# Performance work log

Measured on AMD Instinct MI355X. Metric: run time of the kernel, lower is better.

## Reference

```python
import jax, jax.numpy as jnp
import numpy as np

B, T, C = 2, 1024, 2048
HEAD_SIZE = 64
H = C // HEAD_SIZE          # 32 heads
N_LAYER, LAYER_ID = 24, 12
D_MIX_LORA = 32
LN_EPS = 1e-5


def _layer_norm(x, g, b):
    mu = jnp.mean(x, axis=-1, keepdims=True)
    var = jnp.mean(jnp.square(x - mu), axis=-1, keepdims=True)
    return (x - mu) * jax.lax.rsqrt(var + LN_EPS) * g + b


def setup_inputs() -> dict:
    key = jax.random.key(0)
    ks = jax.random.split(key, 8)
    # data-dependent init of time_maa_* exactly as in the torch module
    r01 = LAYER_ID / (N_LAYER - 1)
    r1a0 = 1.0 - LAYER_ID / N_LAYER
    ddd = np.arange(C, dtype=np.float32) / C
    time_maa_x = jnp.asarray(1.0 - np.power(ddd, r1a0), dtype=jnp.float32)
    time_maa_r = jnp.asarray(1.0 - np.power(ddd, 0.5 * r1a0), dtype=jnp.float32)
    time_maa_k = jnp.asarray(1.0 - np.power(ddd, r1a0), dtype=jnp.float32)
    time_maa_v = jnp.asarray(1.0 - (np.power(ddd, r1a0) + 0.3 * r01), dtype=jnp.float32)
    # LoRA mix weights (w1 is zero-init in the module, keep small random for a nontrivial test)
    w1 = jax.random.uniform(ks[0], (C, D_MIX_LORA * 3), jnp.float32, -0.01, 0.01)
    w2 = jax.random.uniform(ks[1], (3, D_MIX_LORA, C), jnp.float32, -0.01, 0.01)
    scale = 1.0 / np.sqrt(C)
    Wq = jax.random.normal(ks[2], (C, C), jnp.float32) * scale  # stored as [in, out]
    Wk = jax.random.normal(ks[3], (C, C), jnp.float32) * scale
    Wv = jax.random.normal(ks[4], (C, C), jnp.float32) * scale
    Wo = jax.random.normal(ks[5], (C, C), jnp.float32) * scale
    ones = jnp.ones((C,), jnp.float32)
    zeros = jnp.zeros((C,), jnp.float32)
    # rotary angles, standard half-dim frequencies over head_size
    Kd = HEAD_SIZE
    inv_freq = 1.0 / (10000.0 ** (np.arange(0, Kd, 2, dtype=np.float32) / Kd))
    ang = np.outer(np.arange(T, dtype=np.float32), inv_freq)  # [T, Kd//2]
    cos = jnp.asarray(np.cos(ang), jnp.float32)
    sin = jnp.asarray(np.sin(ang), jnp.float32)
    x = jax.random.normal(ks[6], (B, T, C), jnp.float32)
    shift_state = jax.random.normal(ks[7], (B, C), jnp.float32)
    return {
        "x": x, "shift_state": shift_state,
        "time_maa_x": time_maa_x, "time_maa_r": time_maa_r,
        "time_maa_k": time_maa_k, "time_maa_v": time_maa_v,
        "w1": w1, "w2": w2,
        "Wq": Wq, "Wk": Wk, "Wv": Wv, "Wo": Wo,
        "g_r": ones, "b_r": zeros, "g_k": ones, "b_k": zeros,
        "g_v": ones, "b_v": zeros, "g_x": ones, "b_x": zeros,
        "cos": cos, "sin": sin,
    }


def reference(x, shift_state, time_maa_x, time_maa_r, time_maa_k, time_maa_v,
              w1, w2, Wq, Wk, Wv, Wo,
              g_r, b_r, g_k, b_k, g_v, b_v, g_x, b_x, cos, sin):
    Bv, Tv, Cv = x.shape
    Kd = Cv // H
    # token shift: prepend previous-step state, diff against current
    xprev = jnp.concatenate([shift_state[:, None, :], x[:, :-1]], axis=1)
    dxprev = xprev - x
    # data-dependent LoRA mixing coefficients
    xxx = x + dxprev * time_maa_x                      # [B,T,C]
    h = jnp.tanh(xxx @ w1).reshape(Bv, Tv, 3, D_MIX_LORA)
    m = jnp.einsum('btli,lic->lbtc', h, w2)            # [3,B,T,C]
    mr, mk, mv = m[0], m[1], m[2]
    xq = x + dxprev * (time_maa_r + mr)
    xk = x + dxprev * (time_maa_k + mk)
    xv = x + dxprev * (time_maa_v + mv)
    q = _layer_norm(xq @ Wq, g_r, b_r)
    k = _layer_norm(xk @ Wk, g_k, b_k)
    v = _layer_norm(xv @ Wv, g_v, b_v)
    # [B,H,T,K]
    q = q.reshape(Bv, Tv, H, Kd).transpose(0, 2, 1, 3)
    k = k.reshape(Bv, Tv, H, Kd).transpose(0, 2, 1, 3)
    v = v.reshape(Bv, Tv, H, Kd).transpose(0, 2, 1, 3)
    # rotary embedding (half split)
    c = cos[None, None, :, :]
    s = sin[None, None, :, :]
    def rope(t):
        t1, t2 = t[..., :Kd // 2], t[..., Kd // 2:]
        return jnp.concatenate([t1 * c - t2 * s, t1 * s + t2 * c], axis=-1)
    q, k = rope(q), rope(k)
    # causal SDPA
    scores = jnp.einsum('bhtd,bhsd->bhts', q, k) / np.sqrt(Kd)
    mask = jnp.tril(jnp.ones((Tv, Tv), dtype=bool))
    scores = jnp.where(mask, scores, jnp.finfo(scores.dtype).min)
    attn = jax.nn.softmax(scores, axis=-1)
    o = jnp.einsum('bhts,bhsd->bhtd', attn, v)
    o = o.transpose(0, 2, 1, 3).reshape(Bv, Tv, Cv)
    o = _layer_norm(o, g_x, b_x)
    return o @ Wo
```

## Files before the change

kernel.cpp:

```cpp
#include <hip/hip_runtime.h>
#include <math.h>

static constexpr int BB = 2;
static constexpr int TT = 1024;
static constexpr int CC = 2048;
static constexpr int HH = 32;
static constexpr int KD = 64;
static constexpr int BT = BB * TT;

typedef short   v8s  __attribute__((ext_vector_type(8)));
typedef float   v4f  __attribute__((ext_vector_type(4)));
typedef unsigned short u16;
typedef u16     u16x8 __attribute__((ext_vector_type(8)));
typedef u16     u16x4 __attribute__((ext_vector_type(4)));
typedef float   fx4  __attribute__((ext_vector_type(4)));

__device__ __forceinline__ u16 f2bf(float f) {
    unsigned u = __builtin_bit_cast(unsigned, f);
    u = u + 0x7FFFu + ((u >> 16) & 1u);
    return (u16)(u >> 16);
}
__device__ __forceinline__ float bf2f(u16 v) {
    return __builtin_bit_cast(float, ((unsigned)v) << 16);
}

__device__ __forceinline__ void gld16(const u16* g, u16* l) {
    __builtin_amdgcn_global_load_lds(
        (const __attribute__((address_space(1))) void*)g,
        (__attribute__((address_space(3))) void*)l, 16, 0, 0);
}

__device__ __forceinline__ void cstore(float* p, float v) { *p = v; }
__device__ __forceinline__ void cstore(u16* p, float v)   { *p = f2bf(v); }

__global__ __launch_bounds__(256) void k_tconv4(const float* __restrict__ W0,
                                                const float* __restrict__ W1,
                                                const float* __restrict__ W2,
                                                const float* __restrict__ W3,
                                                u16* __restrict__ T0, u16* __restrict__ T1,
                                                u16* __restrict__ T2, u16* __restrict__ T3) {
    int z = blockIdx.z;
    const float* W = (z == 0) ? W0 : (z == 1) ? W1 : (z == 2) ? W2 : W3;
    u16* Wt = (z == 0) ? T0 : (z == 1) ? T1 : (z == 2) ? T2 : T3;
    __shared__ float tile[64][65];
    int tid = threadIdx.x;
    int nb = blockIdx.x * 64, kb = blockIdx.y * 64;
    for (int i = tid; i < 4096; i += 256) {
        int r = i >> 6, c = i & 63;
        tile[r][c] = W[(size_t)(kb + r) * CC + nb + c];
    }
    __syncthreads();
    for (int i = tid; i < 4096; i += 256) {
        int r = i >> 6, c = i & 63;
        Wt[(size_t)(nb + r) * CC + kb + c] = f2bf(tile[c][r]);
    }
}

__global__ __launch_bounds__(256) void k_tconvw1(const float* __restrict__ w1,
                                                 u16* __restrict__ w1t) {
    __shared__ float tile[64][97];
    int tid = threadIdx.x;
    int kb = blockIdx.x * 64;
    for (int i = tid; i < 64 * 96; i += 256) {
        int r = i / 96, c = i - r * 96;
        tile[r][c] = w1[(size_t)(kb + r) * 96 + c];
    }
    __syncthreads();
    for (int i = tid; i < 96 * 64; i += 256) {
        int n = i >> 6, k = i & 63;
        w1t[(size_t)n * CC + kb + k] = f2bf(tile[k][n]);
    }
}

__global__ __launch_bounds__(128) void k_lgemm(const float* __restrict__ x,
                                               const float* __restrict__ shift,
                                               const float* __restrict__ maa_x,
                                               const u16* __restrict__ w1t,
                                               float* __restrict__ h_out) {
    __shared__ u16 As[16 * 64];
    __shared__ u16 Bs[96 * 64];
    int tid = threadIdx.x, lane = tid & 63, wave = tid >> 6;
    int brow = blockIdx.x * 16;

    int ar = tid >> 3, ag = tid & 7;
    int grow = brow + ar;
    int t = grow & (TT - 1), b = grow >> 10;
    const float* xr = x + (size_t)grow * CC;
    const float* xp = (t == 0) ? (shift + (size_t)b * CC) : (xr - CC);
    u16* adst = As + ar * 64 + ((ag ^ (ar & 7)) * 8);

    v4f acc[3];
    #pragma unroll
    for (int ni = 0; ni < 3; ++ni)
        #pragma unroll
        for (int e = 0; e < 4; ++e) acc[ni][e] = 0.f;

    for (int k0 = 0; k0 < CC; k0 += 64) {
        __syncthreads();
        #pragma unroll
        for (int u = 0; u < 6; ++u) {
            int r = (wave * 6 + u) * 8 + (lane >> 3);
            int sc = ((lane & 7) ^ (r & 7)) * 8;
            gld16(w1t + (size_t)r * CC + k0 + sc, Bs + (wave * 6 + u) * 512);
        }
        {
            int kb_ = k0 + ag * 8;
            fx4 x0 = *reinterpret_cast<const fx4*>(xr + kb_);
            fx4 x1 = *reinterpret_cast<const fx4*>(xr + kb_ + 4);
            fx4 p0 = *reinterpret_cast<const fx4*>(xp + kb_);
            fx4 p1 = *reinterpret_cast<const fx4*>(xp + kb_ + 4);
            fx4 m0 = *reinterpret_cast<const fx4*>(maa_x + kb_);
            fx4 m1 = *reinterpret_cast<const fx4*>(maa_x + kb_ + 4);
            fx4 r0 = x0 + (p0 - x0) * m0;
            fx4 r1 = x1 + (p1 - x1) * m1;
            u16x8 a8;
            #pragma unroll
            for (int e = 0; e < 4; ++e) { a8[e] = f2bf(r0[e]); a8[e + 4] = f2bf(r1[e]); }
            *reinterpret_cast<u16x8*>(adst) = a8;
        }
        __syncthreads();

        #pragma unroll
        for (int ks = 0; ks < 2; ++ks) {
            int kg = ks * 4 + (lane >> 4);
            int rlA = lane & 15;
            v8s af = *reinterpret_cast<const v8s*>(As + rlA * 64 + ((kg ^ (rlA & 7)) * 8));
            #pragma unroll
            for (int ni = 0; ni < 3; ++ni) {
                int rlB = wave * 48 + ni * 16 + (lane & 15);
                v8s bf = *reinterpret_cast<const v8s*>(Bs + rlB * 64 + ((kg ^ (rlB & 7)) * 8));
                acc[ni] = __builtin_amdgcn_mfma_f32_16x16x32_bf16(af, bf, acc[ni], 0, 0, 0);
            }
        }
    }

    #pragma unroll
    for (int ni = 0; ni < 3; ++ni) {
        int col = wave * 48 + ni * 16 + (lane & 15);
        #pragma unroll
        for (int j = 0; j < 4; ++j) {
            int row = brow + (lane >> 4) * 4 + j;
            h_out[(size_t)row * 96 + col] = tanhf(acc[ni][j]);
        }
    }
}

__global__ __launch_bounds__(256) void k_mix2(const float* __restrict__ x,
                                              const float* __restrict__ shift,
                                              const float* __restrict__ h_in,
                                              const float* __restrict__ w2,
                                              const float* __restrict__ maa_r,
                                              const float* __restrict__ maa_k,
                                              const float* __restrict__ maa_v,
                                              u16* __restrict__ oq,
                                              u16* __restrict__ ok,
                                              u16* __restrict__ ov) {
    __shared__ float w2s[96][64];
    __shared__ float hs[64][100];
    int tid = threadIdx.x;
    int c0 = blockIdx.x * 64, r0 = blockIdx.y * 64;
    for (int i = tid; i < 96 * 64; i += 256) {
        int r = i >> 6, c = i & 63;
        w2s[r][c] = w2[(size_t)r * CC + c0 + c];
    }
    for (int i = tid; i < 64 * 96; i += 256) {
        int r = i / 96, jj = i - r * 96;
        hs[r][jj] = h_in[(size_t)(r0 + r) * 96 + jj];
    }
    __syncthreads();

    int cq = tid & 15, rg = tid >> 4;
    int c = c0 + cq * 4;
    fx4 acc[4][3];
    #pragma unroll
    for (int r = 0; r < 4; ++r)
        #pragma unroll
        for (int l = 0; l < 3; ++l)
            #pragma unroll
            for (int e = 0; e < 4; ++e) acc[r][l][e] = 0.f;

    #pragma unroll 2
    for (int i4 = 0; i4 < 8; ++i4) {
        fx4 hv[4][3];
        #pragma unroll
        for (int r = 0; r < 4; ++r) {
            int row = rg * 4 + r;
            hv[r][0] = *reinterpret_cast<const fx4*>(&hs[row][i4 * 4]);
            hv[r][1] = *reinterpret_cast<const fx4*>(&hs[row][32 + i4 * 4]);
            hv[r][2] = *reinterpret_cast<const fx4*>(&hs[row][64 + i4 * 4]);
        }
        #pragma unroll
        for (int e = 0; e < 4; ++e) {
            int i = i4 * 4 + e;
            fx4 w0 = *reinterpret_cast<const fx4*>(&w2s[i][cq * 4]);
            fx4 w1v = *reinterpret_cast<const fx4*>(&w2s[32 + i][cq * 4]);
            fx4 w2v = *reinterpret_cast<const fx4*>(&w2s[64 + i][cq * 4]);
            #pragma unroll
            for (int r = 0; r < 4; ++r) {
                acc[r][0] += hv[r][0][e] * w0;
                acc[r][1] += hv[r][1][e] * w1v;
                acc[r][2] += hv[r][2][e] * w2v;
            }
        }
    }

    fx4 m_r = *reinterpret_cast<const fx4*>(maa_r + c);
    fx4 m_k = *reinterpret_cast<const fx4*>(maa_k + c);
    fx4 m_v = *reinterpret_cast<const fx4*>(maa_v + c);
    #pragma unroll
    for (int r = 0; r < 4; ++r) {
        int grow = r0 + rg * 4 + r;
        int t = grow & (TT - 1), b = grow >> 10;
        const float* xr = x + (size_t)grow * CC;
        const float* xp = (t == 0) ? (shift + (size_t)b * CC) : (xr - CC);
        fx4 xv = *reinterpret_cast<const fx4*>(xr + c);
        fx4 pv = *reinterpret_cast<const fx4*>(xp + c);
        fx4 dx = pv - xv;
        fx4 rq = xv + dx * (m_r + acc[r][0]);
        fx4 rk = xv + dx * (m_k + acc[r][1]);
        fx4 rv = xv + dx * (m_v + acc[r][2]);
        u16x4 pq, pk, pvv;
        #pragma unroll
        for (int e = 0; e < 4; ++e) { pq[e] = f2bf(rq[e]); pk[e] = f2bf(rk[e]); pvv[e] = f2bf(rv[e]); }
        size_t o = (size_t)grow * CC + c;
        *reinterpret_cast<u16x4*>(oq + o) = pq;
        *reinterpret_cast<u16x4*>(ok + o) = pk;
        *reinterpret_cast<u16x4*>(ov + o) = pvv;
    }
}

template <typename CT>
__device__ __forceinline__ void gemm_body(const u16* __restrict__ A,
                                          const u16* __restrict__ Bt,
                                          CT* __restrict__ C,
                                          int bm, int bn) {
    constexpr int Kd = 2048, Nd = 2048;
    __shared__ u16 As[128 * 64];
    __shared__ u16 Bs[128 * 64];
    int tid = threadIdx.x;
    int lane = tid & 63, wave = tid >> 6;
    int wr = wave >> 1, wc = wave & 1;

    int srow[4], scol[4];
    #pragma unroll
    for (int q = 0; q < 4; ++q) {
        int e = q * 2048 + wave * 512 + lane * 8;
        int row = e >> 6;
        srow[q] = row;
        scol[q] = ((lane & 7) ^ (row & 7)) * 8;
    }

    v4f acc[4][4];
    #pragma unroll
    for (int i = 0; i < 4; ++i)
        #pragma unroll
        for (int j = 0; j < 4; ++j)
            #pragma unroll
            for (int e = 0; e < 4; ++e) acc[i][j][e] = 0.f;

    for (int k0 = 0; k0 < Kd; k0 += 64) {
        __syncthreads();
        #pragma unroll
        for (int q = 0; q < 4; ++q)
            gld16(A + (size_t)(bm + srow[q]) * Kd + k0 + scol[q], As + q * 2048 + wave * 512);
        #pragma unroll
        for (int q = 0; q < 4; ++q)
            gld16(Bt + (size_t)(bn + srow[q]) * Kd + k0 + scol[q], Bs + q * 2048 + wave * 512);
        __syncthreads();
        #pragma unroll
        for (int ks = 0; ks < 2; ++ks) {
            int kg = ks * 4 + (lane >> 4);
            v8s af[4], bf[4];
            #pragma unroll
            for (int mi = 0; mi < 4; ++mi) {
                int rl = wr * 64 + mi * 16 + (lane & 15);
                af[mi] = *reinterpret_cast<const v8s*>(As + rl * 64 + ((kg ^ (rl & 7)) * 8));
            }
            #pragma unroll
            for (int ni = 0; ni < 4; ++ni) {
                int rl = wc * 64 + ni * 16 + (lane & 15);
                bf[ni] = *reinterpret_cast<const v8s*>(Bs + rl * 64 + ((kg ^ (rl & 7)) * 8));
            }
            #pragma unroll
            for (int mi = 0; mi < 4; ++mi)
                #pragma unroll
                for (int ni = 0; ni < 4; ++ni)
                    acc[mi][ni] = __builtin_amdgcn_mfma_f32_16x16x32_bf16(af[mi], bf[ni], acc[mi][ni], 0, 0, 0);
        }
    }

    int cr = (lane >> 4) * 4;
    int ccol = lane & 15;
    #pragma unroll
    for (int mi = 0; mi < 4; ++mi)
        #pragma unroll
        for (int ni = 0; ni < 4; ++ni) {
            CT* cp = C + (size_t)(bm + wr * 64 + mi * 16 + cr) * Nd + bn + wc * 64 + ni * 16 + ccol;
            #pragma unroll
            for (int j = 0; j < 4; ++j) cstore(cp + (size_t)j * Nd, acc[mi][ni][j]);
        }
}

__global__ __launch_bounds__(256) void k_gemm_qkv(const u16* A0, const u16* A1, const u16* A2,
                                                  const u16* B0, const u16* B1, const u16* B2,
                                                  u16* C0, u16* C1, u16* C2) {
    int z = blockIdx.z;
    const u16* A = (z == 0) ? A0 : (z == 1) ? A1 : A2;
    const u16* B = (z == 0) ? B0 : (z == 1) ? B1 : B2;
    u16* C = (z == 0) ? C0 : (z == 1) ? C1 : C2;
    gemm_body<u16>(A, B, C, blockIdx.y * 128, blockIdx.x * 128);
}

__global__ __launch_bounds__(256) void k_gemm1(const u16* __restrict__ A,
                                               const u16* __restrict__ Bt,
                                               float* __restrict__ C) {
    gemm_body<float>(A, Bt, C, blockIdx.y * 128, blockIdx.x * 128);
}

__global__ __launch_bounds__(256) void k_ln_bb(u16* __restrict__ y, const u16* __restrict__ xin,
                                               const float* __restrict__ g, const float* __restrict__ bb) {
    int row = blockIdx.x;
    const u16* xr = xin + (size_t)row * CC;
    int tid = threadIdx.x;
    u16x8 v8 = *reinterpret_cast<const u16x8*>(xr + tid * 8);
    float xv[8];
    float s = 0.f, ss = 0.f;
    #pragma unroll
    for (int e = 0; e < 8; ++e) { xv[e] = bf2f(v8[e]); s += xv[e]; ss += xv[e] * xv[e]; }
    #pragma unroll
    for (int o = 32; o > 0; o >>= 1) { s += __shfl_xor(s, o); ss += __shfl_xor(ss, o); }
    __shared__ float red[8];
    int wid = tid >> 6;
    if ((tid & 63) == 0) { red[wid] = s; red[wid + 4] = ss; }
    __syncthreads();
    s  = red[0] + red[1] + red[2] + red[3];
    ss = red[4] + red[5] + red[6] + red[7];
    float mu  = s * (1.0f / CC);
    float var = ss * (1.0f / CC) - mu * mu;
    float rsg = rsqrtf(var + 1e-5f);
    fx4 g0 = *reinterpret_cast<const fx4*>(g + tid * 8);
    fx4 g1 = *reinterpret_cast<const fx4*>(g + tid * 8 + 4);
    fx4 b0 = *reinterpret_cast<const fx4*>(bb + tid * 8);
    fx4 b1 = *reinterpret_cast<const fx4*>(bb + tid * 8 + 4);
    u16x8 o8;
    #pragma unroll
    for (int e = 0; e < 4; ++e) o8[e]     = f2bf((xv[e] - mu) * rsg * g0[e] + b0[e]);
    #pragma unroll
    for (int e = 0; e < 4; ++e) o8[e + 4] = f2bf((xv[e + 4] - mu) * rsg * g1[e] + b1[e]);
    *reinterpret_cast<u16x8*>(y + (size_t)row * CC + tid * 8) = o8;
}

__global__ __launch_bounds__(256) void k_lnrope(const u16* __restrict__ qin,
                                                const u16* __restrict__ kin,
                                                u16* __restrict__ qo, u16* __restrict__ ko,
                                                const float* __restrict__ g_r, const float* __restrict__ b_r,
                                                const float* __restrict__ g_k, const float* __restrict__ b_k,
                                                const float* __restrict__ cosb, const float* __restrict__ sinb) {
    int row = blockIdx.x;
    int t = row & (TT - 1);
    int tid = threadIdx.x;
    const u16* qr_ = qin + (size_t)row * CC;
    const u16* kr_ = kin + (size_t)row * CC;
    float sq = 0.f, ssq = 0.f, sk = 0.f, ssk = 0.f;
    {
        u16x8 qv = *reinterpret_cast<const u16x8*>(qr_ + tid * 8);
        u16x8 kv = *reinterpret_cast<const u16x8*>(kr_ + tid * 8);
        #pragma unroll
        for (int e = 0; e < 8; ++e) {
            float qf = bf2f(qv[e]), kf = bf2f(kv[e]);
            sq += qf; ssq += qf * qf;
            sk += kf; ssk += kf * kf;
        }
    }
    #pragma unroll
    for (int o_ = 32; o_ > 0; o_ >>= 1) {
        sq += __shfl_xor(sq, o_); ssq += __shfl_xor(ssq, o_);
        sk += __shfl_xor(sk, o_); ssk += __shfl_xor(ssk, o_);
    }
    __shared__ float red[16];
    int wid = tid >> 6;
    if ((tid & 63) == 0) { red[wid] = sq; red[wid + 4] = ssq; red[wid + 8] = sk; red[wid + 12] = ssk; }
    __syncthreads();
    sq  = red[0] + red[1] + red[2] + red[3];
    ssq = red[4] + red[5] + red[6] + red[7];
    sk  = red[8] + red[9] + red[10] + red[11];
    ssk = red[12] + red[13] + red[14] + red[15];
    float muq = sq * (1.0f / CC), vq = ssq * (1.0f / CC) - muq * muq, rq = rsqrtf(vq + 1e-5f);
    float muk = sk * (1.0f / CC), vk = ssk * (1.0f / CC) - muk * muk, rk = rsqrtf(vk + 1e-5f);
    #pragma unroll
    for (int i = 0; i < 4; ++i) {
        int p = tid + i * 256;
        int h = p >> 5, d = p & 31;
        int c1 = h * 64 + d, c2 = c1 + 32;
        float cv = cosb[t * 32 + d], sv = sinb[t * 32 + d];
        float q1 = (bf2f(qr_[c1]) - muq) * rq * g_r[c1] + b_r[c1];
        float q2 = (bf2f(qr_[c2]) - muq) * rq * g_r[c2] + b_r[c2];
        qo[(size_t)row * CC + c1] = f2bf((q1 * cv - q2 * sv) * 0.125f);
        qo[(size_t)row * CC + c2] = f2bf((q1 * sv + q2 * cv) * 0.125f);
        float k1 = (bf2f(kr_[c1]) - muk) * rk * g_k[c1] + b_k[c1];
        float k2 = (bf2f(kr_[c2]) - muk) * rk * g_k[c2] + b_k[c2];
        ko[(size_t)row * CC + c1] = f2bf(k1 * cv - k2 * sv);
        ko[(size_t)row * CC + c2] = f2bf(k1 * sv + k2 * cv);
    }
}

__global__ __launch_bounds__(256) void k_vtr(const u16* __restrict__ vin,
                                             u16* __restrict__ vout) {
    int t0 = blockIdx.x * 64, h = blockIdx.y, b = blockIdx.z;
    __shared__ u16 tile[64][72];
    int tid = threadIdx.x;
    #pragma unroll
    for (int u = 0; u < 2; ++u) {
        int g = tid + u * 256;
        int r = g >> 3, gc = g & 7;
        u16x8 vv = *reinterpret_cast<const u16x8*>(vin + (size_t)(b * TT + t0 + r) * CC + h * 64 + gc * 8);
        *reinterpret_cast<u16x8*>(&tile[r][gc * 8]) = vv;
    }
    __syncthreads();
    #pragma unroll
    for (int u = 0; u < 2; ++u) {
        int g = tid + u * 256;
        int d = g >> 3, tc = g & 7;
        u16x8 ov;
        #pragma unroll
        for (int e = 0; e < 8; ++e) ov[e] = tile[tc * 8 + e][d];
        *reinterpret_cast<u16x8*>(vout + ((size_t)(b * HH + h) * KD + d) * TT + t0 + tc * 8) = ov;
    }
}

__global__ __launch_bounds__(512) void k_mattn3(const u16* __restrict__ q,
                                                const u16* __restrict__ k,
                                                const u16* __restrict__ vt,
                                                u16* __restrict__ o) {
    int st = (int)gridDim.x - 1 - (int)blockIdx.x;
    int h = blockIdx.y, b = blockIdx.z;
    __shared__ u16 Ks[2][64 * 64];
    __shared__ u16 Vs[2][64 * 64];
    __shared__ u16 Ps[8][16 * 64];
    int tid = threadIdx.x, lane = tid & 63, wave = tid >> 6;
    size_t bh = (size_t)b * TT * CC + (size_t)h * KD;
    const u16* vth = vt + (size_t)(b * HH + h) * KD * TT;
    int qrow0 = st * 128 + wave * 16;

    v8s qf[2];
    {
        const u16* qp = q + bh + (size_t)(qrow0 + (lane & 15)) * CC + (lane >> 4) * 8;
        qf[0] = *reinterpret_cast<const v8s*>(qp);
        qf[1] = *reinterpret_cast<const v8s*>(qp + 32);
    }

    float mstat[4], lstat[4];
    v4f oacc[4];
    #pragma unroll
    for (int j = 0; j < 4; ++j) { mstat[j] = -1e30f; lstat[j] = 0.f; }
    #pragma unroll
    for (int nd = 0; nd < 4; ++nd)
        #pragma unroll
        for (int e = 0; e < 4; ++e) oacc[nd][e] = 0.f;

    int srow = (wave << 3) + (lane >> 3);
    int scol = ((lane & 7) ^ (srow & 7)) << 3;
    u16* pw = Ps[wave];
    int ktmax = 2 * st + 1;

    auto STAGE = [&](int slot, int kt) {
        gld16(k + bh + (size_t)(kt * 64 + srow) * CC + scol, &Ks[slot][wave * 512]);
        gld16(vth + (size_t)srow * TT + kt * 64 + scol, &Vs[slot][wave * 512]);
    };

    STAGE(0, 0);
    STAGE(1, 1);

    for (int kt = 0; kt <= ktmax; ++kt) {
        int cur = kt & 1;
        if (kt < ktmax) asm volatile("s_waitcnt vmcnt(2)" ::: "memory");
        else            asm volatile("s_waitcnt vmcnt(0)" ::: "memory");
        __builtin_amdgcn_s_barrier();
        __builtin_amdgcn_sched_barrier(0);

        if (kt * 64 <= qrow0 + 15) {
            const u16* KsC = Ks[cur];
            const u16* VsC = Vs[cur];

            v4f s[4];
            #pragma unroll
            for (int ni = 0; ni < 4; ++ni) {
                #pragma unroll
                for (int e = 0; e < 4; ++e) s[ni][e] = 0.f;
                #pragma unroll
                for (int ks = 0; ks < 2; ++ks) {
                    int rl = ni * 16 + (lane & 15);
                    int kg = ks * 4 + (lane >> 4);
                    int swz = kg ^ (rl & 7);
                    v8s kf = *reinterpret_cast<const v8s*>(KsC + rl * 64 + swz * 8);
                    s[ni] = __builtin_amdgcn_mfma_f32_16x16x32_bf16(qf[ks], kf, s[ni], 0, 0, 0);
                }
            }
            if (kt * 64 + 63 > qrow0) {
                int qr = qrow0 + (lane >> 4) * 4;
                int kc = kt * 64 + (lane & 15);
                #pragma unroll
                for (int ni = 0; ni < 4; ++ni)
                    #pragma unroll
                    for (int j = 0; j < 4; ++j)
                        if (kc + ni * 16 > qr + j) s[ni][j] = -1e30f;
            }

            float alpha[4];
            #pragma unroll
            for (int j = 0; j < 4; ++j) {
                float pm = fmaxf(fmaxf(s[0][j], s[1][j]), fmaxf(s[2][j], s[3][j]));
                pm = fmaxf(pm, __shfl_xor(pm, 1));
                pm = fmaxf(pm, __shfl_xor(pm, 2));
                pm = fmaxf(pm, __shfl_xor(pm, 4));
                pm = fmaxf(pm, __shfl_xor(pm, 8));
                float mn = fmaxf(mstat[j], pm);
                alpha[j] = __expf(mstat[j] - mn);
                float rs = 0.f;
                #pragma unroll
                for (int ni = 0; ni < 4; ++ni) {
                    float p = __expf(s[ni][j] - mn);
                    s[ni][j] = p;
                    rs += p;
                }
                rs += __shfl_xor(rs, 1);
                rs += __shfl_xor(rs, 2);
                rs += __shfl_xor(rs, 4);
                rs += __shfl_xor(rs, 8);
                lstat[j] = lstat[j] * alpha[j] + rs;
                mstat[j] = mn;
            }
            #pragma unroll
            for (int nd = 0; nd < 4; ++nd)
                #pragma unroll
                for (int j = 0; j < 4; ++j) oacc[nd][j] *= alpha[j];

            #pragma unroll
            for (int ni = 0; ni < 4; ++ni) {
                int kc = (lane & 15) + ni * 16;
                #pragma unroll
                for (int j = 0; j < 4; ++j) {
                    int qr = (lane >> 4) * 4 + j;
                    int swz = (kc >> 3) ^ (qr & 7) ^ (qr >> 3);
                    pw[qr * 64 + swz * 8 + (kc & 7)] = f2bf(s[ni][j]);
                }
            }

            v8s pf[2];
            #pragma unroll
            for (int ks = 0; ks < 2; ++ks) {
                int prow = lane & 15;
                int kg = ks * 4 + (lane >> 4);
                int swz = kg ^ (prow & 7) ^ (prow >> 3);
                pf[ks] = *reinterpret_cast<const v8s*>(pw + prow * 64 + swz * 8);
            }
            #pragma unroll
            for (int nd = 0; nd < 4; ++nd) {
                #pragma unroll
                for (int ks = 0; ks < 2; ++ks) {
                    int vrow = nd * 16 + (lane & 15);
                    int vg = ks * 4 + (lane >> 4);
                    int vswz = vg ^ (vrow & 7);
                    v8s vf = *reinterpret_cast<const v8s*>(VsC + vrow * 64 + vswz * 8);
                    oacc[nd] = __builtin_amdgcn_mfma_f32_16x16x32_bf16(pf[ks], vf, oacc[nd], 0, 0, 0);
                }
            }
        }

        __builtin_amdgcn_sched_barrier(0);
        __builtin_amdgcn_s_barrier();
        if (kt + 2 <= ktmax) STAGE(cur, kt + 2);
    }

    #pragma unroll
    for (int j = 0; j < 4; ++j) {
        int qrow = qrow0 + (lane >> 4) * 4 + j;
        float inv = 1.0f / lstat[j];
        #pragma unroll
        for (int nd = 0; nd < 4; ++nd)
            o[bh + (size_t)qrow * CC + (lane & 15) + nd * 16] = f2bf(oacc[nd][j] * inv);
    }
}

extern "C" void kernel_launch(void* const* d_in, const int* in_sizes, int n_in,
                              void* d_out, int out_size, void* d_ws, size_t ws_size,
                              hipStream_t stream) {
    const float* x     = (const float*)d_in[0];
    const float* shift = (const float*)d_in[1];
    const float* maa_x = (const float*)d_in[2];
    const float* maa_r = (const float*)d_in[3];
    const float* maa_k = (const float*)d_in[4];
    const float* maa_v = (const float*)d_in[5];
    const float* w1    = (const float*)d_in[6];
    const float* w2    = (const float*)d_in[7];
    const float* Wq    = (const float*)d_in[8];
    const float* Wk    = (const float*)d_in[9];
    const float* Wv    = (const float*)d_in[10];
    const float* Wo    = (const float*)d_in[11];
    const float* g_r   = (const float*)d_in[12];
    const float* b_r   = (const float*)d_in[13];
    const float* g_k   = (const float*)d_in[14];
    const float* b_k   = (const float*)d_in[15];
    const float* g_v   = (const float*)d_in[16];
    const float* b_v   = (const float*)d_in[17];
    const float* g_x   = (const float*)d_in[18];
    const float* b_x   = (const float*)d_in[19];
    const float* cosb  = (const float*)d_in[20];
    const float* sinb  = (const float*)d_in[21];

    char* w = (char*)d_ws;
    const size_t WB = (size_t)BT * CC * 2;
    u16*   wtq  = (u16*)(w + 0 * WB);
    u16*   wtk  = (u16*)(w + 1 * WB);
    u16*   wtv  = (u16*)(w + 2 * WB);
    u16*   xqb  = (u16*)(w + 3 * WB);
    u16*   xkb  = (u16*)(w + 4 * WB);
    u16*   xvb  = (u16*)(w + 5 * WB);
    u16*   qb16 = (u16*)(w + 6 * WB);
    u16*   kb16 = (u16*)(w + 7 * WB);
    u16*   vb16 = (u16*)(w + 8 * WB);
    u16*   vtb  = (u16*)(w + 9 * WB);
    float* hb   = (float*)(w + 10 * WB);
    u16*   wto  = (u16*)(w + 11 * WB);
    u16*   w1t  = (u16*)(w + 10 * WB + 4 * 1024 * 1024);
    u16*   qbb = (u16*)(w + 3 * WB);
    u16*   kbb = (u16*)(w + 4 * WB);
    u16*   vbb = (u16*)(w + 5 * WB);
    u16*   ob  = (u16*)(w + 6 * WB);
    u16*   oln = (u16*)(w + 7 * WB);
    float* out = (float*)d_out;

    k_tconvw1<<<32, 256, 0, stream>>>(w1, w1t);
    k_tconv4<<<dim3(32, 32, 4), 256, 0, stream>>>(Wq, Wk, Wv, Wo, wtq, wtk, wtv, wto);

    k_lgemm<<<BT / 16, 128, 0, stream>>>(x, shift, maa_x, w1t, hb);
    k_mix2<<<dim3(32, 32), 256, 0, stream>>>(x, shift, hb, w2, maa_r, maa_k, maa_v,
                                             xqb, xkb, xvb);

    k_gemm_qkv<<<dim3(16, 16, 3), 256, 0, stream>>>(xqb, xkb, xvb, wtq, wtk, wtv,
                                                    qb16, kb16, vb16);

    k_lnrope<<<BT, 256, 0, stream>>>(qb16, kb16, qbb, kbb, g_r, b_r, g_k, b_k, cosb, sinb);
    k_ln_bb<<<BT, 256, 0, stream>>>(vbb, vb16, g_v, b_v);
    k_vtr<<<dim3(TT / 64, HH, BB), 256, 0, stream>>>(vbb, vtb);

    k_mattn3<<<dim3(TT / 128, HH, BB), 512, 0, stream>>>(qbb, kbb, vtb, ob);

    k_ln_bb<<<BT, 256, 0, stream>>>(oln, ob, g_x, b_x);
    k_gemm1<<<dim3(16, 16), 256, 0, stream>>>(oln, wto, out);
}
```

Baseline: 248.8 us.

## Split-K LoRA gemm, fuse transpose kernels, XCD-aware GEMM tiling, MFMA priority hints

Merges the w1 transpose into the weight-transpose kernel, cutting one launch. Splits the small LoRA GEMM four ways over K, with a separate reduction kernel that applies tanh, so more blocks run in parallel. Remaps GEMM block indices so neighbouring tiles land on the same XCD for better L2 reuse. Adds s_setprio around the MFMA sections of attention. The costs are an extra launch and extra partial-sum traffic for the split-K step.

```diff
diff --git a/kernel.cpp b/kernel.cpp
--- a/kernel.cpp
+++ b/kernel.cpp
@@ -33,17 +33,40 @@
 __device__ __forceinline__ void cstore(float* p, float v) { *p = v; }
 __device__ __forceinline__ void cstore(u16* p, float v)   { *p = f2bf(v); }
 
-__global__ __launch_bounds__(256) void k_tconv4(const float* __restrict__ W0,
+__device__ __forceinline__ void xcd_map(int bid, int& bx, int& by) {
+    int i = bid & 7;
+    int j = bid >> 3;
+    bx = (i & 3) * 4 + (j & 3);
+    by = (i >> 2) * 8 + (j >> 2);
+}
+
+__global__ __launch_bounds__(256) void k_tconv5(const float* __restrict__ W0,
                                                 const float* __restrict__ W1,
                                                 const float* __restrict__ W2,
                                                 const float* __restrict__ W3,
+                                                const float* __restrict__ w1,
                                                 u16* __restrict__ T0, u16* __restrict__ T1,
-                                                u16* __restrict__ T2, u16* __restrict__ T3) {
+                                                u16* __restrict__ T2, u16* __restrict__ T3,
+                                                u16* __restrict__ w1t) {
+    __shared__ float tile[64][97];
+    int tid = threadIdx.x;
     int z = blockIdx.z;
+    if (z == 4) {
+        if (blockIdx.y != 0) return;
+        int kb = blockIdx.x * 64;
+        for (int i = tid; i < 64 * 96; i += 256) {
+            int r = i / 96, c = i - r * 96;
+            tile[r][c] = w1[(size_t)(kb + r) * 96 + c];
+        }
+        __syncthreads();
+        for (int i = tid; i < 96 * 64; i += 256) {
+            int n = i >> 6, k = i & 63;
+            w1t[(size_t)n * CC + kb + k] = f2bf(tile[k][n]);
+        }
+        return;
+    }
     const float* W = (z == 0) ? W0 : (z == 1) ? W1 : (z == 2) ? W2 : W3;
     u16* Wt = (z == 0) ? T0 : (z == 1) ? T1 : (z == 2) ? T2 : T3;
-    __shared__ float tile[64][65];
-    int tid = threadIdx.x;
     int nb = blockIdx.x * 64, kb = blockIdx.y * 64;
     for (int i = tid; i < 4096; i += 256) {
         int r = i >> 6, c = i & 63;
@@ -56,31 +79,16 @@
     }
 }
 
-__global__ __launch_bounds__(256) void k_tconvw1(const float* __restrict__ w1,
-                                                 u16* __restrict__ w1t) {
-    __shared__ float tile[64][97];
-    int tid = threadIdx.x;
-    int kb = blockIdx.x * 64;
-    for (int i = tid; i < 64 * 96; i += 256) {
-        int r = i / 96, c = i - r * 96;
-        tile[r][c] = w1[(size_t)(kb + r) * 96 + c];
-    }
-    __syncthreads();
-    for (int i = tid; i < 96 * 64; i += 256) {
-        int n = i >> 6, k = i & 63;
-        w1t[(size_t)n * CC + kb + k] = f2bf(tile[k][n]);
-    }
-}
-
 __global__ __launch_bounds__(128) void k_lgemm(const float* __restrict__ x,
                                                const float* __restrict__ shift,
                                                const float* __restrict__ maa_x,
                                                const u16* __restrict__ w1t,
-                                               float* __restrict__ h_out) {
+                                               float* __restrict__ hp) {
     __shared__ u16 As[16 * 64];
     __shared__ u16 Bs[96 * 64];
     int tid = threadIdx.x, lane = tid & 63, wave = tid >> 6;
     int brow = blockIdx.x * 16;
+    int kbeg = blockIdx.y * 512;
 
     int ar = tid >> 3, ag = tid & 7;
     int grow = brow + ar;
@@ -95,7 +103,7 @@
         #pragma unroll
         for (int e = 0; e < 4; ++e) acc[ni][e] = 0.f;
 
-    for (int k0 = 0; k0 < CC; k0 += 64) {
+    for (int k0 = kbeg; k0 < kbeg + 512; k0 += 64) {
         __syncthreads();
         #pragma unroll
         for (int u = 0; u < 6; ++u) {
@@ -134,15 +142,31 @@
         }
     }
 
+    float* hpk = hp + (size_t)blockIdx.y * BT * 96;
     #pragma unroll
     for (int ni = 0; ni < 3; ++ni) {
         int col = wave * 48 + ni * 16 + (lane & 15);
         #pragma unroll
         for (int j = 0; j < 4; ++j) {
             int row = brow + (lane >> 4) * 4 + j;
-            h_out[(size_t)row * 96 + col] = tanhf(acc[ni][j]);
-        }
-    }
+            hpk[(size_t)row * 96 + col] = acc[ni][j];
+        }
+    }
+}
+
+__global__ __launch_bounds__(256) void k_lred(const float* __restrict__ hp,
+                                              float* __restrict__ h) {
+    int i = (blockIdx.x * 256 + threadIdx.x) * 4;
+    const size_t S = (size_t)BT * 96;
+    fx4 a = *reinterpret_cast<const fx4*>(hp + i);
+    fx4 b = *reinterpret_cast<const fx4*>(hp + S + i);
+    fx4 c = *reinterpret_cast<const fx4*>(hp + 2 * S + i);
+    fx4 d = *reinterpret_cast<const fx4*>(hp + 3 * S + i);
+    fx4 s = a + b + c + d;
+    fx4 o;
+    #pragma unroll
+    for (int e = 0; e < 4; ++e) o[e] = tanhf(s[e]);
+    *reinterpret_cast<fx4*>(h + i) = o;
 }
 
 __global__ __launch_bounds__(256) void k_mix2(const float* __restrict__ x,
@@ -304,17 +328,21 @@
 __global__ __launch_bounds__(256) void k_gemm_qkv(const u16* A0, const u16* A1, const u16* A2,
                                                   const u16* B0, const u16* B1, const u16* B2,
                                                   u16* C0, u16* C1, u16* C2) {
-    int z = blockIdx.z;
+    int z = blockIdx.y;
     const u16* A = (z == 0) ? A0 : (z == 1) ? A1 : A2;
     const u16* B = (z == 0) ? B0 : (z == 1) ? B1 : B2;
     u16* C = (z == 0) ? C0 : (z == 1) ? C1 : C2;
-    gemm_body<u16>(A, B, C, blockIdx.y * 128, blockIdx.x * 128);
+    int bx, by;
+    xcd_map(blockIdx.x, bx, by);
+    gemm_body<u16>(A, B, C, by * 128, bx * 128);
 }
 
 __global__ __launch_bounds__(256) void k_gemm1(const u16* __restrict__ A,
                                                const u16* __restrict__ Bt,
                                                float* __restrict__ C) {
-    gemm_body<float>(A, Bt, C, blockIdx.y * 128, blockIdx.x * 128);
+    int bx, by;
+    xcd_map(blockIdx.x, bx, by);
+    gemm_body<float>(A, Bt, C, by * 128, bx * 128);
 }
 
 __global__ __launch_bounds__(256) void k_ln_bb(u16* __restrict__ y, const u16* __restrict__ xin,
@@ -483,6 +511,7 @@
             const u16* VsC = Vs[cur];
 
             v4f s[4];
+            __builtin_amdgcn_s_setprio(1);
             #pragma unroll
             for (int ni = 0; ni < 4; ++ni) {
                 #pragma unroll
@@ -496,6 +525,7 @@
                     s[ni] = __builtin_amdgcn_mfma_f32_16x16x32_bf16(qf[ks], kf, s[ni], 0, 0, 0);
                 }
             }
+            __builtin_amdgcn_s_setprio(0);
             if (kt * 64 + 63 > qrow0) {
                 int qr = qrow0 + (lane >> 4) * 4;
                 int kc = kt * 64 + (lane & 15);
@@ -554,6 +584,7 @@
                 int swz = kg ^ (prow & 7) ^ (prow >> 3);
                 pf[ks] = *reinterpret_cast<const v8s*>(pw + prow * 64 + swz * 8);
             }
+            __builtin_amdgcn_s_setprio(1);
             #pragma unroll
             for (int nd = 0; nd < 4; ++nd) {
                 #pragma unroll
@@ -565,6 +596,7 @@
                     oacc[nd] = __builtin_amdgcn_mfma_f32_16x16x32_bf16(pf[ks], vf, oacc[nd], 0, 0, 0);
                 }
             }
+            __builtin_amdgcn_s_setprio(0);
         }
 
         __builtin_amdgcn_sched_barrier(0);
@@ -620,9 +652,10 @@
     u16*   kb16 = (u16*)(w + 7 * WB);
     u16*   vb16 = (u16*)(w + 8 * WB);
     u16*   vtb  = (u16*)(w + 9 * WB);
-    float* hb   = (float*)(w + 10 * WB);
+    float* hp   = (float*)(w + 10 * WB);
+    float* hb   = (float*)(w + 10 * WB + 0x300000);
+    u16*   w1t  = (u16*)(w + 10 * WB + 0x400000);
     u16*   wto  = (u16*)(w + 11 * WB);
-    u16*   w1t  = (u16*)(w + 10 * WB + 4 * 1024 * 1024);
     u16*   qbb = (u16*)(w + 3 * WB);
     u16*   kbb = (u16*)(w + 4 * WB);
     u16*   vbb = (u16*)(w + 5 * WB);
@@ -630,15 +663,16 @@
     u16*   oln = (u16*)(w + 7 * WB);
     float* out = (float*)d_out;
 
-    k_tconvw1<<<32, 256, 0, stream>>>(w1, w1t);
-    k_tconv4<<<dim3(32, 32, 4), 256, 0, stream>>>(Wq, Wk, Wv, Wo, wtq, wtk, wtv, wto);
-
-    k_lgemm<<<BT / 16, 128, 0, stream>>>(x, shift, maa_x, w1t, hb);
+    k_tconv5<<<dim3(32, 32, 5), 256, 0, stream>>>(Wq, Wk, Wv, Wo, w1,
+                                                  wtq, wtk, wtv, wto, w1t);
+
+    k_lgemm<<<dim3(BT / 16, 4), 128, 0, stream>>>(x, shift, maa_x, w1t, hp);
+    k_lred<<<BT * 96 / 1024, 256, 0, stream>>>(hp, hb);
     k_mix2<<<dim3(32, 32), 256, 0, stream>>>(x, shift, hb, w2, maa_r, maa_k, maa_v,
                                              xqb, xkb, xvb);
 
-    k_gemm_qkv<<<dim3(16, 16, 3), 256, 0, stream>>>(xqb, xkb, xvb, wtq, wtk, wtv,
-                                                    qb16, kb16, vb16);
+    k_gemm_qkv<<<dim3(256, 3), 256, 0, stream>>>(xqb, xkb, xvb, wtq, wtk, wtv,
+                                                 qb16, kb16, vb16);
 
     k_lnrope<<<BT, 256, 0, stream>>>(qb16, kb16, qbb, kbb, g_r, b_r, g_k, b_k, cosb, sinb);
     k_ln_bb<<<BT, 256, 0, stream>>>(vbb, vb16, g_v, b_v);
@@ -647,5 +681,5 @@
     k_mattn3<<<dim3(TT / 128, HH, BB), 512, 0, stream>>>(qbb, kbb, vtb, ob);
 
     k_ln_bb<<<BT, 256, 0, stream>>>(oln, ob, g_x, b_x);
-    k_gemm1<<<dim3(16, 16), 256, 0, stream>>>(oln, wto, out);
-}
+    k_gemm1<<<256, 256, 0, stream>>>(oln, wto, out);
+}
```

Result: faster. 231.3 us (-7.0%).
